# Kernel tuning notes

Measured on AMD Instinct MI355X. Metric: run time of the kernel, lower is better.

## Reference

```python
import jax, jax.numpy as jnp
import numpy as np

R_CUT = 5.0
N_NODES = 50000
N_EDGES = 400000
N_GRAPHS = 2500
D = 128        # embedding_size (hardcoded by torch.split(..., 128))
N_RBF = 20
N_BLOCKS = 3
PI = 3.141592653589793


def setup_inputs() -> dict:
    key = jax.random.key(0)
    ks = jax.random.split(key, 32)
    w = lambda k, s: (jax.random.normal(k, s) * 0.05).astype(jnp.float32)
    z = jax.random.randint(ks[0], (N_NODES,), 0, 100)
    edges = jax.random.randint(ks[1], (N_EDGES, 2), 0, N_NODES)
    r_ij = jax.random.uniform(ks[2], (N_EDGES, 1), minval=0.8, maxval=R_CUT, dtype=jnp.float32)
    d = jax.random.normal(ks[3], (N_EDGES, 3), dtype=jnp.float32)
    r_ij_normalized = d / jnp.linalg.norm(d, axis=1, keepdims=True)
    graph_idx = jax.random.randint(ks[4], (N_NODES,), 0, N_GRAPHS)
    return {
        "z": z, "edges": edges, "r_ij": r_ij,
        "r_ij_normalized": r_ij_normalized, "graph_idx": graph_idx,
        "emb": w(ks[5], (100, D)),
        # message blocks (stacked over N_BLOCKS)
        "msg_w1": w(ks[6], (N_BLOCKS, D, D)),   "msg_b1": w(ks[7], (N_BLOCKS, D)),
        "msg_w2": w(ks[8], (N_BLOCKS, D, 3 * D)), "msg_b2": w(ks[9], (N_BLOCKS, 3 * D)),
        "rbf_w": w(ks[10], (N_BLOCKS, N_RBF, 3 * D)), "rbf_b": w(ks[11], (N_BLOCKS, 3 * D)),
        # update blocks
        "upd_U": w(ks[12], (N_BLOCKS, D, D)), "upd_V": w(ks[13], (N_BLOCKS, D, D)),
        "upd_w1": w(ks[14], (N_BLOCKS, 2 * D, D)), "upd_b1": w(ks[15], (N_BLOCKS, D)),
        "upd_w2": w(ks[16], (N_BLOCKS, D, 3 * D)), "upd_b2": w(ks[17], (N_BLOCKS, 3 * D)),
        # readout
        "blue_w1": w(ks[18], (D, D)), "blue_b1": w(ks[19], (D,)),
        "blue_w2": w(ks[20], (D, 1)), "blue_b2": w(ks[21], (1,)),
    }


def _rbf(r, r_cut):
    n = jnp.arange(1, N_RBF + 1, dtype=r.dtype)  # [20]
    return jnp.sin(n * PI / r_cut * r) / r        # [E,20]


def _fcut(r, r_cut):
    return jnp.where(r <= r_cut, 0.5 * (jnp.cos(PI * r / r_cut) + 1.0), 0.0)


def painn_forward(z, edges, r_ij, r_ij_normalized, graph_idx, emb,
                  msg_w1, msg_b1, msg_w2, msg_b2, rbf_w, rbf_b,
                  upd_U, upd_V, upd_w1, upd_b1, upd_w2, upd_b2,
                  blue_w1, blue_b1, blue_w2, blue_b2):
    silu = jax.nn.silu
    src = edges[:, 1]  # gathered (neighbor j)
    dst = edges[:, 0]  # scattered (center i)
    s = emb[z]                                           # [N,128]
    v = jnp.zeros((s.shape[0], 3, D), dtype=r_ij.dtype)  # [N,3,128]
    rbf = _rbf(r_ij, R_CUT)                              # [E,20]
    f_c = _fcut(r_ij, R_CUT)                             # [E,1]
    for i in range(N_BLOCKS):
        # --- message block ---
        rbf_fcut = (rbf @ rbf_w[i] + rbf_b[i]) * f_c            # [E,384]
        s_pass = silu(s @ msg_w1[i] + msg_b1[i]) @ msg_w2[i] + msg_b2[i]  # [N,384]
        pass_out = rbf_fcut * s_pass[src]                        # [E,384]
        d_v, d_s, d_rep = jnp.split(pass_out, 3, axis=-1)        # each [E,128]
        delta_v = v[src] * d_v[:, None, :] + r_ij_normalized[:, :, None] * d_rep[:, None, :]
        s = s + jax.ops.segment_sum(d_s, dst, num_segments=N_NODES)
        v = v + jax.ops.segment_sum(delta_v, dst, num_segments=N_NODES)
        # --- update block ---
        U_v = jnp.einsum('nde,ef->ndf', v, upd_U[i])             # [N,3,128]
        V_v = jnp.einsum('nde,ef->ndf', v, upd_V[i])
        V_norm = jnp.linalg.norm(V_v, axis=1)                    # [N,128]
        sv = jnp.concatenate([V_norm, s], axis=1)                # [N,256]
        a = silu(sv @ upd_w1[i] + upd_b1[i]) @ upd_w2[i] + upd_b2[i]  # [N,384]
        avv, asv, ass = jnp.split(a, 3, axis=1)
        s = s + jnp.sum(U_v * V_v, axis=1) * asv + ass
        v = v + avv[:, None, :] * U_v
    blue = silu(s @ blue_w1 + blue_b1) @ blue_w2 + blue_b2       # [N,1]
    return jax.ops.segment_sum(blue, graph_idx, num_segments=N_GRAPHS)  # [G,1]


def reference(z, edges, r_ij, r_ij_normalized, graph_idx, emb,
              msg_w1, msg_b1, msg_w2, msg_b2, rbf_w, rbf_b,
              upd_U, upd_V, upd_w1, upd_b1, upd_w2, upd_b2,
              blue_w1, blue_b1, blue_w2, blue_b2):
    return painn_forward(z, edges, r_ij, r_ij_normalized, graph_idx, emb,
                         msg_w1, msg_b1, msg_w2, msg_b2, rbf_w, rbf_b,
                         upd_U, upd_V, upd_w1, upd_b1, upd_w2, upd_b2,
                         blue_w1, blue_b1, blue_w2, blue_b2)
```

## Files before the change

### kernel.cpp

```cpp
#include <hip/hip_runtime.h>
#include <hip/hip_bf16.h>
#include <math.h>

#define N_NODES 50000
#define N_EDGES 400000
#define N_GRAPHS 2500
#define D 128
#define D3 384
#define N_RBF 20
#define R_CUT 5.0f
#define PI_F 3.14159265358979f
#define GEB 16
#define GLDS_STRIDE 388

typedef __attribute__((ext_vector_type(8))) short bf16x8;
typedef __attribute__((ext_vector_type(4))) float f32x4;

__device__ __forceinline__ float silu_f(float x) {
    return x / (1.0f + __expf(-x));
}
__device__ __forceinline__ short f2bf(float x) {
    union { float f; unsigned u; } v; v.f = x;
    unsigned r = (v.u + 0x7FFFu + ((v.u >> 16) & 1u)) >> 16;
    return (short)r;
}
__device__ __forceinline__ float bf2f(short x) {
    union { unsigned u; float f; } v; v.u = ((unsigned)(unsigned short)x) << 16;
    return v.f;
}
__device__ __forceinline__ float bflo(unsigned u) {
    union { unsigned x; float f; } v; v.x = u << 16; return v.f;
}
__device__ __forceinline__ float bfhi(unsigned u) {
    union { unsigned x; float f; } v; v.x = u & 0xFFFF0000u; return v.f;
}
__device__ __forceinline__ unsigned packbf(float a, float b) {
    return ((unsigned)(unsigned short)f2bf(a)) | (((unsigned)(unsigned short)f2bf(b)) << 16);
}

#define MAXJOBS 19
struct PackJobs {
    const float* W[MAXJOBS];
    short* P[MAXJOBS];
    int K[MAXJOBS];
    int N[MAXJOBS];
    int boff[MAXJOBS + 1];
    int njobs;
};
__global__ void k_packall(PackJobs jobs) {
    int b = blockIdx.x;
    int j = 0;
    while (j + 1 < jobs.njobs && b >= jobs.boff[j + 1]) ++j;
    int t = (b - jobs.boff[j]) * 256 + threadIdx.x;
    int K = jobs.K[j], N = jobs.N[j];
    int NKT = K / 32;
    int total = (N / 16) * NKT * 64;
    if (t >= total) return;
    const float* W = jobs.W[j];
    short* P = jobs.P[j];
    int lane = t & 63;
    int kt = (t >> 6) % NKT;
    int nt = (t >> 6) / NKT;
    int k0 = kt * 32 + (lane >> 4) * 8;
    int col = nt * 16 + (lane & 15);
    #pragma unroll
    for (int q = 0; q < 8; ++q)
        P[(size_t)t * 8 + q] = f2bf(W[(size_t)(k0 + q) * N + col]);
}

__global__ void k_packrbf(const float* __restrict__ rbf_w, const float* __restrict__ rbf_b,
                          short* __restrict__ P) {
    int t = blockIdx.x * 256 + threadIdx.x;
    if (t >= 3 * 1536) return;
    int i = t / 1536;
    int r = t - i * 1536;
    int lane = r & 63;
    int nt = r >> 6;
    int col = nt * 16 + (lane & 15);
    int k0 = (lane >> 4) * 8;
    const float* W = rbf_w + (size_t)i * N_RBF * D3;
    const float* B = rbf_b + (size_t)i * D3;
    short* out = P + (size_t)i * 12288 + (size_t)r * 8;
    #pragma unroll
    for (int q = 0; q < 8; ++q) {
        int k = k0 + q;
        float v = (k < N_RBF) ? W[(size_t)k * D3 + col] : ((k == N_RBF) ? B[col] : 0.0f);
        out[q] = f2bf(v);
    }
}

template<int K, int N, bool SILU, int AMODE>
__global__ __launch_bounds__(256) void k_gemm(const void* __restrict__ Aptr,
                                              const void* __restrict__ A2ptr,
                                              const short* __restrict__ Bp,
                                              const float* __restrict__ bias,
                                              short* __restrict__ Cbf, int M) {
    constexpr int NKT = K / 32, NNT = N / 16;
    int lane = threadIdx.x & 63, wv = threadIdx.x >> 6;
    int tile = blockIdx.x * 4 + wv;
    int base = tile * 32;
    if (base >= M) return;
    bool has2 = (base + 16 < M);
    int r16 = lane & 15;
    int kgrp = (lane >> 4) * 8;
    int arow0 = base + r16;
    int arow1 = has2 ? (base + 16 + r16) : arow0;

    bf16x8 a0[NKT], a1[NKT];
    #pragma unroll
    for (int ss = 0; ss < 2; ++ss) {
        int arow = ss ? arow1 : arow0;
        bf16x8* a = ss ? a1 : a0;
        if (AMODE == 0) {
            const short* A = (const short*)Aptr + (size_t)arow * K + kgrp;
            #pragma unroll
            for (int kt = 0; kt < NKT; ++kt) a[kt] = *(const bf16x8*)(A + kt * 32);
        } else if (AMODE == 1) {
            const float* A = (const float*)Aptr + (size_t)arow * K + kgrp;
            #pragma unroll
            for (int kt = 0; kt < NKT; ++kt)
                #pragma unroll
                for (int j = 0; j < 8; ++j) a[kt][j] = f2bf(A[kt * 32 + j]);
        } else {
            const short* A1 = (const short*)Aptr + (size_t)arow * D3 + kgrp;
            const float* A2 = (const float*)A2ptr + (size_t)arow * 128 + kgrp;
            #pragma unroll
            for (int kt = 0; kt < 4 && kt < NKT; ++kt) {
                bf16x8 v0 = *(const bf16x8*)(A1 + kt * 32);
                bf16x8 v1 = *(const bf16x8*)(A1 + kt * 32 + 128);
                bf16x8 v2 = *(const bf16x8*)(A1 + kt * 32 + 256);
                #pragma unroll
                for (int j = 0; j < 8; ++j) {
                    float f0 = bf2f(v0[j]), f1 = bf2f(v1[j]), f2 = bf2f(v2[j]);
                    a[kt][j] = f2bf(sqrtf(f0 * f0 + f1 * f1 + f2 * f2));
                }
            }
            #pragma unroll
            for (int kt = 4; kt < NKT; ++kt)
                #pragma unroll
                for (int j = 0; j < 8; ++j) a[kt][j] = f2bf(A2[(kt - 4) * 32 + j]);
        }
    }

    int crow0 = base + (lane >> 4) * 4;
    int ccol = lane & 15;
    const bf16x8* Bv = (const bf16x8*)Bp;
    #pragma unroll
    for (int nt = 0; nt < NNT; ++nt) {
        f32x4 acc0 = {0.f, 0.f, 0.f, 0.f};
        f32x4 acc1 = {0.f, 0.f, 0.f, 0.f};
        #pragma unroll
        for (int kt = 0; kt < NKT; ++kt) {
            bf16x8 b = Bv[(nt * NKT + kt) * 64 + lane];
            acc0 = __builtin_amdgcn_mfma_f32_16x16x32_bf16(a0[kt], b, acc0, 0, 0, 0);
            acc1 = __builtin_amdgcn_mfma_f32_16x16x32_bf16(a1[kt], b, acc1, 0, 0, 0);
        }
        int col = nt * 16 + ccol;
        float bs = bias ? bias[col] : 0.0f;
        #pragma unroll
        for (int j = 0; j < 4; ++j) {
            float v = acc0[j] + bs;
            if (SILU) v = silu_f(v);
            Cbf[(size_t)(crow0 + j) * N + col] = f2bf(v);
        }
        if (has2) {
            #pragma unroll
            for (int j = 0; j < 4; ++j) {
                float v = acc1[j] + bs;
                if (SILU) v = silu_f(v);
                Cbf[(size_t)(crow0 + 16 + j) * N + col] = f2bf(v);
            }
        }
    }
}

__global__ __launch_bounds__(256) void k_gemmUV(const short* __restrict__ A,
                                                const short* __restrict__ Bp,
                                                short* __restrict__ Cu,
                                                short* __restrict__ Cv, int M) {
    int lane = threadIdx.x & 63, wv = threadIdx.x >> 6;
    int tile = blockIdx.x * 4 + wv;
    int base = tile * 32;
    if (base >= M) return;
    bool has2 = (base + 16 < M);
    int r16 = lane & 15;
    int kgrp = (lane >> 4) * 8;
    const short* Ar0 = A + (size_t)(base + r16) * 128 + kgrp;
    const short* Ar1 = A + (size_t)((has2 ? base + 16 : base) + r16) * 128 + kgrp;
    bf16x8 a0[4], a1[4];
    #pragma unroll
    for (int kt = 0; kt < 4; ++kt) {
        a0[kt] = *(const bf16x8*)(Ar0 + kt * 32);
        a1[kt] = *(const bf16x8*)(Ar1 + kt * 32);
    }
    int crow0 = base + (lane >> 4) * 4;
    int ccol = lane & 15;
    const bf16x8* Bv = (const bf16x8*)Bp;
    #pragma unroll
    for (int nt = 0; nt < 16; ++nt) {
        f32x4 acc0 = {0.f, 0.f, 0.f, 0.f};
        f32x4 acc1 = {0.f, 0.f, 0.f, 0.f};
        #pragma unroll
        for (int kt = 0; kt < 4; ++kt) {
            bf16x8 b = Bv[(nt * 4 + kt) * 64 + lane];
            acc0 = __builtin_amdgcn_mfma_f32_16x16x32_bf16(a0[kt], b, acc0, 0, 0, 0);
            acc1 = __builtin_amdgcn_mfma_f32_16x16x32_bf16(a1[kt], b, acc1, 0, 0, 0);
        }
        int col = nt * 16 + ccol;
        short* C = (col < 128) ? Cu : Cv;
        int cc = col & 127;
        #pragma unroll
        for (int j = 0; j < 4; ++j)
            C[(size_t)(crow0 + j) * 128 + cc] = f2bf(acc0[j]);
        if (has2) {
            #pragma unroll
            for (int j = 0; j < 4; ++j)
                C[(size_t)(crow0 + 16 + j) * 128 + cc] = f2bf(acc1[j]);
        }
    }
}

__global__ __launch_bounds__(256) void k_bluefused(const float* __restrict__ s,
                                                   const short* __restrict__ Bp,
                                                   const float* __restrict__ b1,
                                                   const float* __restrict__ w2,
                                                   const float* __restrict__ b2,
                                                   const int* __restrict__ graph_idx,
                                                   float* __restrict__ out, int M) {
    int lane = threadIdx.x & 63, wv = threadIdx.x >> 6;
    int tile = blockIdx.x * 4 + wv;
    int base = tile * 32;
    if (base >= M) return;
    bool has2 = (base + 16 < M);
    int r16 = lane & 15;
    int kgrp = (lane >> 4) * 8;
    int arow0 = base + r16;
    int arow1 = has2 ? (base + 16 + r16) : arow0;
    bf16x8 a0[4], a1[4];
    {
        const float* A = s + (size_t)arow0 * 128 + kgrp;
        #pragma unroll
        for (int kt = 0; kt < 4; ++kt)
            #pragma unroll
            for (int j = 0; j < 8; ++j) a0[kt][j] = f2bf(A[kt * 32 + j]);
        const float* B = s + (size_t)arow1 * 128 + kgrp;
        #pragma unroll
        for (int kt = 0; kt < 4; ++kt)
            #pragma unroll
            for (int j = 0; j < 8; ++j) a1[kt][j] = f2bf(B[kt * 32 + j]);
    }
    int crow0 = base + (lane >> 4) * 4;
    int ccol = lane & 15;
    const bf16x8* Bv = (const bf16x8*)Bp;
    float dot0[4] = {0.f, 0.f, 0.f, 0.f};
    float dot1[4] = {0.f, 0.f, 0.f, 0.f};
    #pragma unroll
    for (int nt = 0; nt < 8; ++nt) {
        f32x4 acc0 = {0.f, 0.f, 0.f, 0.f};
        f32x4 acc1 = {0.f, 0.f, 0.f, 0.f};
        #pragma unroll
        for (int kt = 0; kt < 4; ++kt) {
            bf16x8 b = Bv[(nt * 4 + kt) * 64 + lane];
            acc0 = __builtin_amdgcn_mfma_f32_16x16x32_bf16(a0[kt], b, acc0, 0, 0, 0);
            acc1 = __builtin_amdgcn_mfma_f32_16x16x32_bf16(a1[kt], b, acc1, 0, 0, 0);
        }
        int col = nt * 16 + ccol;
        float bs = b1[col], w = w2[col];
        #pragma unroll
        for (int j = 0; j < 4; ++j) {
            dot0[j] += silu_f(acc0[j] + bs) * w;
            dot1[j] += silu_f(acc1[j] + bs) * w;
        }
    }
    #pragma unroll
    for (int m = 1; m <= 8; m <<= 1) {
        #pragma unroll
        for (int j = 0; j < 4; ++j) {
            dot0[j] += __shfl_xor(dot0[j], m, 64);
            dot1[j] += __shfl_xor(dot1[j], m, 64);
        }
    }
    if (ccol == 0) {
        #pragma unroll
        for (int j = 0; j < 4; ++j) {
            int n = crow0 + j;
            atomicAdd(&out[graph_idx[n]], dot0[j] + b2[0]);
        }
        if (has2) {
            #pragma unroll
            for (int j = 0; j < 4; ++j) {
                int n = crow0 + 16 + j;
                atomicAdd(&out[graph_idx[n]], dot1[j] + b2[0]);
            }
        }
    }
}

__global__ void k_embed(const int* __restrict__ z, const float* __restrict__ emb,
                        float* __restrict__ s) {
    int i = blockIdx.x * blockDim.x + threadIdx.x;
    if (i < N_NODES * D) {
        int n = i >> 7, c = i & 127;
        s[i] = emb[z[n] * D + c];
    }
}

__global__ void k_hist(const int* __restrict__ edges, int* __restrict__ cnt) {
    int e = blockIdx.x * 256 + threadIdx.x;
    if (e < N_EDGES) atomicAdd(&cnt[edges[2 * e]], 1);
}

#define SCH 49
__global__ __launch_bounds__(1024) void k_scanall(int* __restrict__ cnt,
                                                  int* __restrict__ rowptr) {
    __shared__ int part[1024];
    int t = threadIdx.x;
    int lo = t * SCH;
    int hi = lo + SCH; if (hi > N_NODES) hi = N_NODES;
    int sum = 0;
    for (int i = lo; i < hi; ++i) sum += cnt[i];
    part[t] = sum;
    __syncthreads();
    for (int off = 1; off < 1024; off <<= 1) {
        int v = (t >= off) ? part[t - off] : 0;
        __syncthreads();
        part[t] += v;
        __syncthreads();
    }
    int run = part[t] - sum;
    for (int i = lo; i < hi; ++i) {
        rowptr[i] = run;
        run += cnt[i];
        cnt[i] = 0;
    }
    if (t == 1023) rowptr[N_NODES] = N_EDGES;
}

__global__ void k_scatter(const int* __restrict__ edges, const float* __restrict__ r_ij,
                          const float* __restrict__ rhat, const int* __restrict__ rowptr,
                          int* __restrict__ cursor, int* __restrict__ esrc,
                          short* __restrict__ erbf, float4* __restrict__ erhat) {
    int e = blockIdx.x * 256 + threadIdx.x;
    if (e >= N_EDGES) return;
    int dst = edges[2 * e], src = edges[2 * e + 1];
    int p = rowptr[dst] + atomicAdd(&cursor[dst], 1);
    esrc[p] = src;
    float r = r_ij[e];
    float fc = (r <= R_CUT) ? 0.5f * (cosf(PI_F * r / R_CUT) + 1.0f) : 0.0f;
    float inv_r = 1.0f / r;
    short rec[32];
    #pragma unroll
    for (int k = 0; k < N_RBF; ++k)
        rec[k] = f2bf(sinf((float)(k + 1) * (PI_F / R_CUT) * r) * inv_r * fc);
    rec[20] = f2bf(fc);
    #pragma unroll
    for (int k = 21; k < 32; ++k) rec[k] = 0;
    short* out = erbf + (size_t)p * 32;
    #pragma unroll
    for (int k = 0; k < 32; ++k) out[k] = rec[k];
    float4 rh;
    rh.x = rhat[3 * e]; rh.y = rhat[3 * e + 1]; rh.z = rhat[3 * e + 2]; rh.w = 0.f;
    erhat[p] = rh;
}

template<bool HASV>
__global__ __launch_bounds__(128, 4) void k_edge4(
    const int* __restrict__ rowptr, const int* __restrict__ esrc,
    const short* __restrict__ erbf, const float4* __restrict__ erhat,
    const short* __restrict__ pRbf,
    const short* __restrict__ spass, const short* __restrict__ vold,
    float* __restrict__ s, short* __restrict__ vnew) {
    __shared__ short gate_lds[GEB * GLDS_STRIDE];
    __shared__ int   src_lds[GEB];
    __shared__ float4 rh_lds[GEB];
    __shared__ float red[64 * 9];
    int tid = threadIdx.x;
    int lane = tid & 63;
    int wv = tid >> 6;
    int ntb = wv * 12;
    int c0 = lane * 2;
    bf16x8 bfr[12];
    #pragma unroll
    for (int t = 0; t < 12; ++t)
        bfr[t] = *(const bf16x8*)(pRbf + ((size_t)((ntb + t) * 64 + lane)) * 8);
    int r0 = (lane >> 4) * 4;
    int fcol = lane & 15;
    for (int n = blockIdx.x; n < N_NODES; n += gridDim.x) {
        int p0 = rowptr[n], p1 = rowptr[n + 1];
        float sa0 = 0.f, sa1 = 0.f;
        float va00 = 0.f, va01 = 0.f, va10 = 0.f, va11 = 0.f, va20 = 0.f, va21 = 0.f;
        for (int pb = p0; pb < p1; pb += GEB) {
            int erow = pb + (lane & 15);
            if (erow >= p1) erow = p1 - 1;
            bf16x8 afrag = *(const bf16x8*)(erbf + (size_t)erow * 32 + (lane >> 4) * 8);
            if (tid < GEB) {
                int p = pb + tid;
                if (p < p1) { src_lds[tid] = esrc[p]; rh_lds[tid] = erhat[p]; }
            }
            #pragma unroll
            for (int t = 0; t < 12; ++t) {
                f32x4 acc = {0.f, 0.f, 0.f, 0.f};
                acc = __builtin_amdgcn_mfma_f32_16x16x32_bf16(afrag, bfr[t], acc, 0, 0, 0);
                int col = (ntb + t) * 16 + fcol;
                #pragma unroll
                for (int j = 0; j < 4; ++j)
                    gate_lds[(r0 + j) * GLDS_STRIDE + col] = f2bf(acc[j]);
            }
            __syncthreads();
            int pe = (pb + GEB < p1) ? pb + GEB : p1;
            for (int p = pb + wv; p < pe; p += 2) {
                int src = src_lds[p - pb];
                float4 rh = rh_lds[p - pb];
                const short* g = gate_lds + (p - pb) * GLDS_STRIDE;
                unsigned ga1 = *(const unsigned*)(g + 128 + c0);
                unsigned ga2 = *(const unsigned*)(g + 256 + c0);
                const short* sp = spass + (size_t)src * D3;
                unsigned sp1 = *(const unsigned*)(sp + 128 + c0);
                unsigned sp2 = *(const unsigned*)(sp + 256 + c0);
                sa0 += bflo(ga1) * bflo(sp1);
                sa1 += bfhi(ga1) * bfhi(sp1);
                float drl = bflo(ga2) * bflo(sp2);
                float drh = bfhi(ga2) * bfhi(sp2);
                if (HASV) {
                    unsigned ga0 = *(const unsigned*)(g + c0);
                    unsigned sp0 = *(const unsigned*)(sp + c0);
                    float dvl = bflo(ga0) * bflo(sp0);
                    float dvh = bfhi(ga0) * bfhi(sp0);
                    const short* vs = vold + (size_t)src * D3;
                    unsigned v0 = *(const unsigned*)(vs + c0);
                    unsigned v1 = *(const unsigned*)(vs + 128 + c0);
                    unsigned v2 = *(const unsigned*)(vs + 256 + c0);
                    va00 += bflo(v0) * dvl + rh.x * drl;
                    va01 += bfhi(v0) * dvh + rh.x * drh;
                    va10 += bflo(v1) * dvl + rh.y * drl;
                    va11 += bfhi(v1) * dvh + rh.y * drh;
                    va20 += bflo(v2) * dvl + rh.z * drl;
                    va21 += bfhi(v2) * dvh + rh.z * drh;
                } else {
                    va00 += rh.x * drl; va01 += rh.x * drh;
                    va10 += rh.y * drl; va11 += rh.y * drh;
                    va20 += rh.z * drl; va21 += rh.z * drh;
                }
            }
            __syncthreads();
        }
        float* rl = red + lane * 9;
        __syncthreads();
        if (wv == 1) {
            rl[0] = sa0; rl[1] = sa1;
            rl[2] = va00; rl[3] = va01; rl[4] = va10; rl[5] = va11; rl[6] = va20; rl[7] = va21;
        }
        __syncthreads();
        if (wv == 0) {
            sa0 += rl[0]; sa1 += rl[1];
            va00 += rl[2]; va01 += rl[3]; va10 += rl[4]; va11 += rl[5]; va20 += rl[6]; va21 += rl[7];
            float2 sv = *(float2*)(s + (size_t)n * D + c0);
            sv.x += sa0; sv.y += sa1;
            *(float2*)(s + (size_t)n * D + c0) = sv;
            size_t vb = (size_t)n * D3;
            if (HASV) {
                unsigned o0 = *(const unsigned*)(vold + vb + c0);
                unsigned o1 = *(const unsigned*)(vold + vb + 128 + c0);
                unsigned o2 = *(const unsigned*)(vold + vb + 256 + c0);
                va00 += bflo(o0); va01 += bfhi(o0);
                va10 += bflo(o1); va11 += bfhi(o1);
                va20 += bflo(o2); va21 += bfhi(o2);
            }
            *(unsigned*)(vnew + vb + c0)       = packbf(va00, va01);
            *(unsigned*)(vnew + vb + 128 + c0) = packbf(va10, va11);
            *(unsigned*)(vnew + vb + 256 + c0) = packbf(va20, va21);
        }
    }
}

__global__ void k_apply(float* __restrict__ s, short* __restrict__ v,
                        const short* __restrict__ Uv, const short* __restrict__ Vv,
                        const short* __restrict__ a_bf) {
    int i = blockIdx.x * 256 + threadIdx.x;
    int n = i >> 6, c0 = (i & 63) * 2;
    size_t ab = (size_t)n * D3;
    unsigned avv = *(const unsigned*)(a_bf + ab + c0);
    unsigned asv = *(const unsigned*)(a_bf + ab + 128 + c0);
    unsigned ass = *(const unsigned*)(a_bf + ab + 256 + c0);
    float scal0 = 0.f, scal1 = 0.f;
    float u0[3], u1[3];
    #pragma unroll
    for (int d = 0; d < 3; ++d) {
        unsigned uu = *(const unsigned*)(Uv + ab + d * 128 + c0);
        unsigned vv = *(const unsigned*)(Vv + ab + d * 128 + c0);
        u0[d] = bflo(uu); u1[d] = bfhi(uu);
        scal0 += u0[d] * bflo(vv);
        scal1 += u1[d] * bfhi(vv);
    }
    float2 sv = *(float2*)(s + (size_t)n * D + c0);
    sv.x += scal0 * bflo(asv) + bflo(ass);
    sv.y += scal1 * bfhi(asv) + bfhi(ass);
    *(float2*)(s + (size_t)n * D + c0) = sv;
    float a0 = bflo(avv), a1 = bfhi(avv);
    #pragma unroll
    for (int d = 0; d < 3; ++d) {
        unsigned* vp = (unsigned*)(v + ab + d * 128 + c0);
        unsigned old = *vp;
        *vp = packbf(bflo(old) + a0 * u0[d], bfhi(old) + a1 * u1[d]);
    }
}

static inline int g32(int M) { int t = (M + 31) / 32; return (t + 3) / 4; }

extern "C" void kernel_launch(void* const* d_in, const int* in_sizes, int n_in,
                              void* d_out, int out_size, void* d_ws, size_t ws_size,
                              hipStream_t stream) {
    const int*   z         = (const int*)d_in[0];
    const int*   edges     = (const int*)d_in[1];
    const float* r_ij      = (const float*)d_in[2];
    const float* rhat      = (const float*)d_in[3];
    const int*   graph_idx = (const int*)d_in[4];
    const float* emb       = (const float*)d_in[5];
    const float* msg_w1    = (const float*)d_in[6];
    const float* msg_b1    = (const float*)d_in[7];
    const float* msg_w2    = (const float*)d_in[8];
    const float* msg_b2    = (const float*)d_in[9];
    const float* rbf_w     = (const float*)d_in[10];
    const float* rbf_b     = (const float*)d_in[11];
    const float* upd_U     = (const float*)d_in[12];
    const float* upd_V     = (const float*)d_in[13];
    const float* upd_w1    = (const float*)d_in[14];
    const float* upd_b1    = (const float*)d_in[15];
    const float* upd_w2    = (const float*)d_in[16];
    const float* upd_b2    = (const float*)d_in[17];
    const float* blue_w1   = (const float*)d_in[18];
    const float* blue_b1   = (const float*)d_in[19];
    const float* blue_w2   = (const float*)d_in[20];
    const float* blue_b2   = (const float*)d_in[21];
    float* out = (float*)d_out;

    char* ws = (char*)d_ws;
    size_t off = 0;
    auto alloc = [&](size_t bytes) { void* p = ws + off; off += (bytes + 255) & ~(size_t)255; return p; };

    float* s      = (float*)alloc((size_t)N_NODES * D * 4);
    short* bufV0  = (short*)alloc((size_t)N_NODES * D3 * 2);
    short* bufV1  = (short*)alloc((size_t)N_NODES * D3 * 2);
    short* shrd   = (short*)alloc((size_t)N_NODES * D3 * 2);
    short* hbuf   = (short*)alloc((size_t)N_NODES * D * 2);
    short* Vv     = (short*)alloc((size_t)N_NODES * D3 * 2);
    int*    esrc   = (int*)alloc((size_t)N_EDGES * 4);
    short*  erbf   = (short*)alloc((size_t)N_EDGES * 32 * 2);
    float4* erhat  = (float4*)alloc((size_t)N_EDGES * 16);
    int*    rowptr = (int*)alloc((size_t)(N_NODES + 1) * 4);
    int*    cnt    = (int*)alloc((size_t)N_NODES * 4);

    short* pBlue = (short*)alloc(16384 * 2);
    short* pRbfAll = (short*)alloc((size_t)3 * 12288 * 2);
    short* pMsgW1[3]; short* pMsgW2[3]; short* pUV[3]; short* pUpdW1[3]; short* pUpdW2[3];
    for (int i = 0; i < 3; ++i) {
        pMsgW1[i] = (short*)alloc(16384 * 2);
        pMsgW2[i] = (short*)alloc(49152 * 2);
        pUV[i]    = (short*)alloc(32768 * 2);
        pUpdW1[i] = (short*)alloc(32768 * 2);
        pUpdW2[i] = (short*)alloc(49152 * 2);
    }

    PackJobs jobs;
    jobs.njobs = 0;
    int bacc = 0;
    auto addjob = [&](const float* W, short* P, int K, int N) {
        int j = jobs.njobs++;
        jobs.W[j] = W; jobs.P[j] = P; jobs.K[j] = K; jobs.N[j] = N;
        jobs.boff[j] = bacc;
        int total = (N / 16) * (K / 32) * 64;
        bacc += (total + 255) / 256;
        jobs.boff[j + 1] = bacc;
    };
    addjob(blue_w1, pBlue, 128, 128);
    for (int i = 0; i < 3; ++i) {
        addjob(msg_w1 + (size_t)i * D * D,     pMsgW1[i], 128, 128);
        addjob(msg_w2 + (size_t)i * D * D3,    pMsgW2[i], 128, 384);
        addjob(upd_U  + (size_t)i * D * D,     pUV[i],          128, 128);
        addjob(upd_V  + (size_t)i * D * D,     pUV[i] + 16384,  128, 128);
        addjob(upd_w1 + (size_t)i * 2 * D * D, pUpdW1[i], 256, 128);
        addjob(upd_w2 + (size_t)i * D * D3,    pUpdW2[i], 128, 384);
    }
    k_packall<<<bacc, 256, 0, stream>>>(jobs);
    k_packrbf<<<18, 256, 0, stream>>>(rbf_w, rbf_b, pRbfAll);

    hipMemsetAsync(cnt, 0, (size_t)N_NODES * 4, stream);
    k_hist<<<(N_EDGES + 255) / 256, 256, 0, stream>>>(edges, cnt);
    k_scanall<<<1, 1024, 0, stream>>>(cnt, rowptr);
    k_scatter<<<(N_EDGES + 255) / 256, 256, 0, stream>>>(edges, r_ij, rhat, rowptr, cnt,
                                                         esrc, erbf, erhat);

    hipMemsetAsync(d_out, 0, (size_t)out_size * sizeof(float), stream);
    k_embed<<<(N_NODES * D) / 256, 256, 0, stream>>>(z, emb, s);

    const int gN  = g32(N_NODES);
    const int gN3 = g32(N_NODES * 3);

    for (int i = 0; i < 3; ++i) {
        short* vstate = (i & 1) ? bufV1 : bufV0;
        short* vscr   = (i & 1) ? bufV0 : bufV1;
        k_gemm<128, 128, true, 1><<<gN, 256, 0, stream>>>(
            s, nullptr, pMsgW1[i], msg_b1 + (size_t)i * D, hbuf, N_NODES);
        k_gemm<128, 384, false, 0><<<gN, 256, 0, stream>>>(
            hbuf, nullptr, pMsgW2[i], msg_b2 + (size_t)i * D3, shrd, N_NODES);
        if (i == 0)
            k_edge4<false><<<4096, 128, 0, stream>>>(rowptr, esrc, erbf, erhat,
                                                     pRbfAll, shrd, vstate, s, vscr);
        else
            k_edge4<true><<<4096, 128, 0, stream>>>(rowptr, esrc, erbf, erhat,
                                                    pRbfAll + (size_t)i * 12288,
                                                    shrd, vstate, s, vscr);
        k_gemmUV<<<gN3, 256, 0, stream>>>(vscr, pUV[i], vstate, Vv, N_NODES * 3);
        k_gemm<256, 128, true, 3><<<gN, 256, 0, stream>>>(
            Vv, s, pUpdW1[i], upd_b1 + (size_t)i * D, hbuf, N_NODES);
        k_gemm<128, 384, false, 0><<<gN, 256, 0, stream>>>(
            hbuf, nullptr, pUpdW2[i], upd_b2 + (size_t)i * D3, shrd, N_NODES);
        k_apply<<<(N_NODES * 64) / 256, 256, 0, stream>>>(s, vscr, vstate, Vv, shrd);
    }

    k_bluefused<<<gN, 256, 0, stream>>>(s, pBlue, blue_b1, blue_w2, blue_b2,
                                        graph_idx, out, N_NODES);
}
```

Measured before the change: 1.054 ms.

## Split node GEMMs across output-column blocks and precompute vector norms separately

The node-level GEMMs now use a second grid dimension that divides the output column tiles among 2 or 3 blocks. This raises the number of waves in flight at the cost of reloading the A rows once per split. The update GEMM no longer computes the norm of Vv while loading A. A new k_svbuild kernel writes the norms into a bf16 buffer that aliases shrd, which adds a launch and an extra pass over memory but leaves the GEMM prologue simpler. The AMODE 3 call is changed to template mode 2, which shares the same else-branch.

```diff
diff --git a/kernel.cpp b/kernel.cpp
--- a/kernel.cpp
+++ b/kernel.cpp
@@ -89,13 +89,13 @@
     }
 }
 
-template<int K, int N, bool SILU, int AMODE>
+template<int K, int N, bool SILU, int AMODE, int SPLIT>
 __global__ __launch_bounds__(256) void k_gemm(const void* __restrict__ Aptr,
                                               const void* __restrict__ A2ptr,
                                               const short* __restrict__ Bp,
                                               const float* __restrict__ bias,
                                               short* __restrict__ Cbf, int M) {
-    constexpr int NKT = K / 32, NNT = N / 16;
+    constexpr int NKT = K / 32, NNT = N / 16, NNTB = NNT / SPLIT;
     int lane = threadIdx.x & 63, wv = threadIdx.x >> 6;
     int tile = blockIdx.x * 4 + wv;
     int base = tile * 32;
@@ -122,19 +122,10 @@
                 #pragma unroll
                 for (int j = 0; j < 8; ++j) a[kt][j] = f2bf(A[kt * 32 + j]);
         } else {
-            const short* A1 = (const short*)Aptr + (size_t)arow * D3 + kgrp;
+            const short* A1 = (const short*)Aptr + (size_t)arow * 128 + kgrp;
             const float* A2 = (const float*)A2ptr + (size_t)arow * 128 + kgrp;
             #pragma unroll
-            for (int kt = 0; kt < 4 && kt < NKT; ++kt) {
-                bf16x8 v0 = *(const bf16x8*)(A1 + kt * 32);
-                bf16x8 v1 = *(const bf16x8*)(A1 + kt * 32 + 128);
-                bf16x8 v2 = *(const bf16x8*)(A1 + kt * 32 + 256);
-                #pragma unroll
-                for (int j = 0; j < 8; ++j) {
-                    float f0 = bf2f(v0[j]), f1 = bf2f(v1[j]), f2 = bf2f(v2[j]);
-                    a[kt][j] = f2bf(sqrtf(f0 * f0 + f1 * f1 + f2 * f2));
-                }
-            }
+            for (int kt = 0; kt < 4 && kt < NKT; ++kt) a[kt] = *(const bf16x8*)(A1 + kt * 32);
             #pragma unroll
             for (int kt = 4; kt < NKT; ++kt)
                 #pragma unroll
@@ -144,9 +135,11 @@
 
     int crow0 = base + (lane >> 4) * 4;
     int ccol = lane & 15;
+    int nt0 = blockIdx.y * NNTB;
     const bf16x8* Bv = (const bf16x8*)Bp;
     #pragma unroll
-    for (int nt = 0; nt < NNT; ++nt) {
+    for (int t = 0; t < NNTB; ++t) {
+        int nt = nt0 + t;
         f32x4 acc0 = {0.f, 0.f, 0.f, 0.f};
         f32x4 acc1 = {0.f, 0.f, 0.f, 0.f};
         #pragma unroll
@@ -473,6 +466,18 @@
     }
 }
 
+__global__ void k_svbuild(const short* __restrict__ Vv, short* __restrict__ Vn) {
+    int i = blockIdx.x * 256 + threadIdx.x;
+    int n = i >> 7, c = i & 127;
+    float acc = 0.f;
+    #pragma unroll
+    for (int d = 0; d < 3; ++d) {
+        float v = bf2f(Vv[(size_t)(n * 3 + d) * D + c]);
+        acc += v * v;
+    }
+    Vn[i] = f2bf(sqrtf(acc));
+}
+
 __global__ void k_apply(float* __restrict__ s, short* __restrict__ v,
                         const short* __restrict__ Uv, const short* __restrict__ Vv,
                         const short* __restrict__ a_bf) {
@@ -544,6 +549,7 @@
     short* shrd   = (short*)alloc((size_t)N_NODES * D3 * 2);
     short* hbuf   = (short*)alloc((size_t)N_NODES * D * 2);
     short* Vv     = (short*)alloc((size_t)N_NODES * D3 * 2);
+    short* Vn     = shrd;
     int*    esrc   = (int*)alloc((size_t)N_EDGES * 4);
     short*  erbf   = (short*)alloc((size_t)N_EDGES * 32 * 2);
     float4* erhat  = (float4*)alloc((size_t)N_EDGES * 16);
@@ -599,9 +605,9 @@
     for (int i = 0; i < 3; ++i) {
         short* vstate = (i & 1) ? bufV1 : bufV0;
         short* vscr   = (i & 1) ? bufV0 : bufV1;
-        k_gemm<128, 128, true, 1><<<gN, 256, 0, stream>>>(
+        k_gemm<128, 128, true, 1, 2><<<dim3(gN, 2), 256, 0, stream>>>(
             s, nullptr, pMsgW1[i], msg_b1 + (size_t)i * D, hbuf, N_NODES);
-        k_gemm<128, 384, false, 0><<<gN, 256, 0, stream>>>(
+        k_gemm<128, 384, false, 0, 3><<<dim3(gN, 3), 256, 0, stream>>>(
             hbuf, nullptr, pMsgW2[i], msg_b2 + (size_t)i * D3, shrd, N_NODES);
         if (i == 0)
             k_edge4<false><<<4096, 128, 0, stream>>>(rowptr, esrc, erbf, erhat,
@@ -611,9 +617,10 @@
                                                     pRbfAll + (size_t)i * 12288,
                                                     shrd, vstate, s, vscr);
         k_gemmUV<<<gN3, 256, 0, stream>>>(vscr, pUV[i], vstate, Vv, N_NODES * 3);
-        k_gemm<256, 128, true, 3><<<gN, 256, 0, stream>>>(
-            Vv, s, pUpdW1[i], upd_b1 + (size_t)i * D, hbuf, N_NODES);
-        k_gemm<128, 384, false, 0><<<gN, 256, 0, stream>>>(
+        k_svbuild<<<(N_NODES * D) / 256, 256, 0, stream>>>(Vv, Vn);
+        k_gemm<256, 128, true, 2, 2><<<dim3(gN, 2), 256, 0, stream>>>(
+            Vn, s, pUpdW1[i], upd_b1 + (size_t)i * D, hbuf, N_NODES);
+        k_gemm<128, 384, false, 0, 3><<<dim3(gN, 3), 256, 0, stream>>>(
             hbuf, nullptr, pUpdW2[i], upd_b2 + (size_t)i * D3, shrd, N_NODES);
         k_apply<<<(N_NODES * 64) / 256, 256, 0, stream>>>(s, vscr, vstate, Vv, shrd);
     }
```

New measurement: 1.063 ms. About the same (+0.9%).
